# Kernel optimization log

Measured on AMD Instinct MI355X. Metric: run time of the kernel, lower is better.

Reference implementation:

```python
import jax, jax.numpy as jnp
import numpy as np

N = 100000      # nodes
E = 3200000     # directed edges (avg degree 32)
F_IN, HID, CLS = 512, 256, 64


def setup_inputs() -> dict:
    key = jax.random.key(0)
    k = jax.random.split(key, 6)
    x = jax.random.normal(k[0], (N, F_IN), dtype=jnp.float32)
    edge_index = jax.random.randint(k[1], (2, E), 0, N, dtype=jnp.int32)
    W1 = jax.random.normal(k[2], (F_IN, HID), dtype=jnp.float32) / np.float32(np.sqrt(F_IN))
    b1 = jnp.zeros((HID,), dtype=jnp.float32)
    W2 = jax.random.normal(k[3], (HID, CLS), dtype=jnp.float32) / np.float32(np.sqrt(HID))
    b2 = jnp.zeros((CLS,), dtype=jnp.float32)
    return {"x": x, "edge_index": edge_index, "W1": W1, "b1": b1, "W2": W2, "b2": b2}


def gcn_layer(x, W, b, src, dst, n):
    """GCN layer: out = D^{-1/2} (A + I) D^{-1/2} (x W + b)."""
    h = x @ W + b                                   # [n, out]
    loop = jnp.arange(n, dtype=src.dtype)
    s = jnp.concatenate([src, loop])                # add self loops
    d = jnp.concatenate([dst, loop])
    deg = jax.ops.segment_sum(jnp.ones_like(d, dtype=h.dtype), d, num_segments=n)
    dinv = jax.lax.rsqrt(jnp.maximum(deg, 1.0))
    norm = dinv[s] * dinv[d]                        # [E+n]
    return jax.ops.segment_sum(h[s] * norm[:, None], d, num_segments=n)


def reference(x, edge_index, W1, b1, W2, b2):
    src, dst = edge_index[0], edge_index[1]
    n = x.shape[0]
    h = jax.nn.relu(gcn_layer(x, W1, b1, src, dst, n))
    # dropout is identity in eval mode
    h = gcn_layer(h, W2, b2, src, dst, n)
    return jax.nn.log_softmax(h, axis=1)
```

## Files before the change

### kernel.cpp

```cpp
#include <hip/hip_runtime.h>

#define FIN 512
#define HID 256
#define CLS 64
#define PAD 8
#define BKT_SLACK 4096

typedef short bf16x8 __attribute__((ext_vector_type(8)));
typedef float f32x4 __attribute__((ext_vector_type(4)));
typedef float f32x2 __attribute__((ext_vector_type(2)));

__device__ __forceinline__ float bf2f(unsigned short u) {
    union { unsigned int i; float f; } c; c.i = ((unsigned int)u) << 16; return c.f;
}
__device__ __forceinline__ unsigned short f2bf(float f) {
    union { float f; unsigned int u; } c; c.f = f;
    unsigned int u = c.u;
    return (unsigned short)((u + 0x7fffu + ((u >> 16) & 1u)) >> 16);
}
__device__ __forceinline__ unsigned char f2fp8(float v) {
    int r = __builtin_amdgcn_cvt_pk_fp8_f32(v, v, 0, false);
    return (unsigned char)(r & 0xFF);
}


__global__ __launch_bounds__(256) void k_hist(const int* __restrict__ dst,
                                              int* __restrict__ bktcnt, int E) {
    __shared__ int h[256];
    h[threadIdx.x] = 0;
    __syncthreads();
    for (int i = blockIdx.x * blockDim.x + threadIdx.x; i < E; i += gridDim.x * blockDim.x)
        atomicAdd(&h[dst[i] >> 9], 1);
    __syncthreads();
    if (h[threadIdx.x]) atomicAdd(&bktcnt[threadIdx.x], h[threadIdx.x]);
}

__global__ __launch_bounds__(256) void k_bktscan(const int* __restrict__ bktcnt,
                                                 int* __restrict__ bkt_base,
                                                 int* __restrict__ bkt_cursor,
                                                 int NB, int E) {
    __shared__ int sh[256];
    int t = threadIdx.x;
    int v = (t < NB) ? bktcnt[t] : 0;
    sh[t] = v;
    __syncthreads();
    for (int s = 1; s < 256; s <<= 1) {
        int u = (t >= s) ? sh[t - s] : 0;
        __syncthreads();
        sh[t] += u;
        __syncthreads();
    }
    int excl = sh[t] - v;
    if (t < NB) { bkt_base[t] = excl; bkt_cursor[t] = excl; }
    if (t == 0) bkt_base[NB] = E;
}

#define EPB 4096
__global__ __launch_bounds__(256) void k_binscatter(
        const int* __restrict__ src, const int* __restrict__ dst,
        int* __restrict__ bkt_cursor, uint2* __restrict__ ebuf, int E) {
    __shared__ int h[256];
    __shared__ int cb[256];
    int t = threadIdx.x;
    h[t] = 0;
    __syncthreads();
    int base = blockIdx.x * EPB;
    int es[16], ed[16], lp[16];
    #pragma unroll
    for (int it = 0; it < 16; ++it) {
        int i = base + it * 256 + t;
        if (i < E) {
            es[it] = src[i];
            ed[it] = dst[i];
            lp[it] = atomicAdd(&h[ed[it] >> 9], 1);
        } else {
            es[it] = -1; ed[it] = 0; lp[it] = 0;
        }
    }
    __syncthreads();
    int c = h[t];
    if (c) cb[t] = atomicAdd(&bkt_cursor[t], c);
    __syncthreads();
    #pragma unroll
    for (int it = 0; it < 16; ++it) {
        if (es[it] >= 0) {
            int b = ed[it] >> 9;
            ebuf[cb[b] + lp[it]] = make_uint2((unsigned)es[it], (unsigned)ed[it]);
        }
    }
}

__global__ __launch_bounds__(256) void k_csrbuild(
        const uint2* __restrict__ ebuf, const int* __restrict__ bkt_base,
        int* __restrict__ rs, int* __restrict__ cnte, float* __restrict__ dinv,
        int* __restrict__ csr, int Nn) {
    __shared__ int deg[512];
    __shared__ int cur[512];
    __shared__ int ts[256];
    int b = blockIdx.x, t = threadIdx.x;
    int e0 = bkt_base[b], e1 = bkt_base[b + 1];
    int pb = e0 + b * BKT_SLACK;
    int node0 = b << 9;
    deg[t] = 0; deg[t + 256] = 0;
    __syncthreads();
    for (int j = e0 + t; j < e1; j += 256)
        atomicAdd(&deg[(int)ebuf[j].y - node0], 1);
    __syncthreads();
    int n0 = node0 + 2 * t;
    int d0 = deg[2 * t], d1 = deg[2 * t + 1];
    int p0 = (n0 < Nn)     ? ((d0 + 1 + PAD - 1) & ~(PAD - 1)) : 0;
    int p1 = (n0 + 1 < Nn) ? ((d1 + 1 + PAD - 1) & ~(PAD - 1)) : 0;
    ts[t] = p0 + p1;
    __syncthreads();
    for (int s = 1; s < 256; s <<= 1) {
        int u = (t >= s) ? ts[t - s] : 0;
        __syncthreads();
        ts[t] += u;
        __syncthreads();
    }
    int excl = ts[t] - (p0 + p1);
    cur[2 * t] = excl;
    cur[2 * t + 1] = excl + p0;
    if (n0 < Nn)     { rs[n0]     = pb + excl;      cnte[n0]     = p0; dinv[n0]     = rsqrtf((float)(d0 + 1)); }
    if (n0 + 1 < Nn) { rs[n0 + 1] = pb + excl + p0; cnte[n0 + 1] = p1; dinv[n0 + 1] = rsqrtf((float)(d1 + 1)); }
    __syncthreads();
    for (int j = e0 + t; j < e1; j += 256) {
        uint2 e = ebuf[j];
        int p = atomicAdd(&cur[(int)e.y - node0], 1);
        csr[pb + p] = (int)e.x;
    }
    if (n0 < Nn) {
        csr[pb + excl + d0] = n0;
        for (int j = d0 + 1; j < p0; ++j) csr[pb + excl + j] = Nn;
    }
    if (n0 + 1 < Nn) {
        csr[pb + excl + p0 + d1] = n0 + 1;
        for (int j = d1 + 1; j < p1; ++j) csr[pb + excl + p0 + j] = Nn;
    }
}

__global__ void k_wpack(const float* __restrict__ W, unsigned short* __restrict__ Wp,
                        int K, int Ncols) {
    int i = blockIdx.x * blockDim.x + threadIdx.x;
    if (i < K * Ncols) {
        int k = i / Ncols, n = i - k * Ncols;
        Wp[((size_t)(k >> 3) * Ncols + n) * 8 + (k & 7)] = f2bf(W[i]);
    }
}

__global__ __launch_bounds__(512) void k_gemm1(
        const float* __restrict__ x, const unsigned short* __restrict__ W1p,
        const float* __restrict__ b1, const float* __restrict__ dinv,
        unsigned char* __restrict__ hs1, int Nn) {
    __shared__ unsigned short As[64][40];
    int tid = threadIdx.x;
    int w = tid >> 6, lane = tid & 63;
    int wr = w >> 2, wc = w & 3;
    int l15 = lane & 15, l4 = lane >> 4;
    int row0 = blockIdx.x * 64;

    f32x4 zero = {0.f, 0.f, 0.f, 0.f};
    f32x4 acc[2][4];
    #pragma unroll
    for (int m = 0; m < 2; ++m)
        #pragma unroll
        for (int n = 0; n < 4; ++n) acc[m][n] = zero;

    int sr = tid >> 3;
    int sc = tid & 7;
    bool srok = (row0 + sr) < Nn;
    const float* xrow = x + (size_t)(row0 + sr) * FIN + sc * 4;

    for (int kt = 0; kt < FIN; kt += 32) {
        float4 v = srok ? *(const float4*)(xrow + kt) : make_float4(0.f, 0.f, 0.f, 0.f);
        ushort4 o;
        o.x = f2bf(v.x); o.y = f2bf(v.y); o.z = f2bf(v.z); o.w = f2bf(v.w);
        *(ushort4*)&As[sr][sc * 4] = o;
        __syncthreads();

        bf16x8 bfr[4];
        size_t bbase = (size_t)((kt >> 3) + l4) * HID * 8;
        #pragma unroll
        for (int n = 0; n < 4; ++n) {
            int col = wc * 64 + n * 16 + l15;
            bfr[n] = *(const bf16x8*)&W1p[bbase + (size_t)col * 8];
        }
        bf16x8 afr[2];
        #pragma unroll
        for (int m = 0; m < 2; ++m) {
            int r = wr * 32 + m * 16 + l15;
            afr[m] = *(const bf16x8*)&As[r][l4 * 8];
        }
        #pragma unroll
        for (int m = 0; m < 2; ++m)
            #pragma unroll
            for (int n = 0; n < 4; ++n)
                acc[m][n] = __builtin_amdgcn_mfma_f32_16x16x32_bf16(
                    afr[m], bfr[n], acc[m][n], 0, 0, 0);
        __syncthreads();
    }

    float b1c[4];
    #pragma unroll
    for (int n = 0; n < 4; ++n) b1c[n] = b1[wc * 64 + n * 16 + l15];
    #pragma unroll
    for (int m = 0; m < 2; ++m) {
        #pragma unroll
        for (int r = 0; r < 4; ++r) {
            int row = row0 + wr * 32 + m * 16 + l4 * 4 + r;
            if (row < Nn) {
                float dv = dinv[row];
                #pragma unroll
                for (int n = 0; n < 4; ++n) {
                    int col = wc * 64 + n * 16 + l15;
                    hs1[(size_t)row * HID + col] = f2fp8((acc[m][n][r] + b1c[n]) * dv);
                }
            }
        }
    }
}

__global__ __launch_bounds__(256) void k_agg1(
        const unsigned char* __restrict__ hs1, const int* __restrict__ csr,
        const int* __restrict__ rs, const int* __restrict__ cnte,
        const float* __restrict__ dinv, unsigned short* __restrict__ h2in, int Nn) {
    int d = blockIdx.x * 4 + (threadIdx.x >> 6);
    if (d >= Nn) return;
    int lane = threadIdx.x & 63;
    int g = lane >> 4, c = lane & 15;
    size_t coff = (size_t)c * 16;
    float acc[16];
    #pragma unroll
    for (int j = 0; j < 16; ++j) acc[j] = 0.f;
    int base = rs[d], cnt = cnte[d];
    const int* cp = csr + base;
    int t = 0;
    for (; t + 16 <= cnt; t += 16) {
        int i0 = cp[t + g], i1 = cp[t + 4 + g], i2 = cp[t + 8 + g], i3 = cp[t + 12 + g];
        uint4 v0 = *(const uint4*)&hs1[(size_t)i0 * HID + coff];
        uint4 v1 = *(const uint4*)&hs1[(size_t)i1 * HID + coff];
        uint4 v2 = *(const uint4*)&hs1[(size_t)i2 * HID + coff];
        uint4 v3 = *(const uint4*)&hs1[(size_t)i3 * HID + coff];
        unsigned int w0[4] = {v0.x, v0.y, v0.z, v0.w};
        unsigned int w1[4] = {v1.x, v1.y, v1.z, v1.w};
        unsigned int w2[4] = {v2.x, v2.y, v2.z, v2.w};
        unsigned int w3[4] = {v3.x, v3.y, v3.z, v3.w};
        #pragma unroll
        for (int k = 0; k < 4; ++k) {
            f32x2 a0 = __builtin_amdgcn_cvt_pk_f32_fp8(w0[k], false);
            f32x2 b0 = __builtin_amdgcn_cvt_pk_f32_fp8(w0[k], true);
            f32x2 a1 = __builtin_amdgcn_cvt_pk_f32_fp8(w1[k], false);
            f32x2 b1v = __builtin_amdgcn_cvt_pk_f32_fp8(w1[k], true);
            f32x2 a2 = __builtin_amdgcn_cvt_pk_f32_fp8(w2[k], false);
            f32x2 b2v = __builtin_amdgcn_cvt_pk_f32_fp8(w2[k], true);
            f32x2 a3 = __builtin_amdgcn_cvt_pk_f32_fp8(w3[k], false);
            f32x2 b3 = __builtin_amdgcn_cvt_pk_f32_fp8(w3[k], true);
            acc[k*4+0] += (a0[0] + a1[0]) + (a2[0] + a3[0]);
            acc[k*4+1] += (a0[1] + a1[1]) + (a2[1] + a3[1]);
            acc[k*4+2] += (b0[0] + b1v[0]) + (b2v[0] + b3[0]);
            acc[k*4+3] += (b0[1] + b1v[1]) + (b2v[1] + b3[1]);
        }
    }
    if (t < cnt) {
        int i0 = cp[t + g], i1 = cp[t + 4 + g];
        uint4 v0 = *(const uint4*)&hs1[(size_t)i0 * HID + coff];
        uint4 v1 = *(const uint4*)&hs1[(size_t)i1 * HID + coff];
        unsigned int w0[4] = {v0.x, v0.y, v0.z, v0.w};
        unsigned int w1[4] = {v1.x, v1.y, v1.z, v1.w};
        #pragma unroll
        for (int k = 0; k < 4; ++k) {
            f32x2 a0 = __builtin_amdgcn_cvt_pk_f32_fp8(w0[k], false);
            f32x2 b0 = __builtin_amdgcn_cvt_pk_f32_fp8(w0[k], true);
            f32x2 a1 = __builtin_amdgcn_cvt_pk_f32_fp8(w1[k], false);
            f32x2 b1v = __builtin_amdgcn_cvt_pk_f32_fp8(w1[k], true);
            acc[k*4+0] += a0[0] + a1[0];
            acc[k*4+1] += a0[1] + a1[1];
            acc[k*4+2] += b0[0] + b1v[0];
            acc[k*4+3] += b0[1] + b1v[1];
        }
    }
    #pragma unroll
    for (int j = 0; j < 16; ++j) {
        acc[j] += __shfl_xor(acc[j], 16);
        acc[j] += __shfl_xor(acc[j], 32);
    }
    float dv = dinv[d];
    ushort4 o;
    o.x = f2bf(fmaxf(acc[g * 4 + 0] * dv, 0.f));
    o.y = f2bf(fmaxf(acc[g * 4 + 1] * dv, 0.f));
    o.z = f2bf(fmaxf(acc[g * 4 + 2] * dv, 0.f));
    o.w = f2bf(fmaxf(acc[g * 4 + 3] * dv, 0.f));
    *(ushort4*)&h2in[(size_t)d * HID + c * 16 + g * 4] = o;
}

__global__ __launch_bounds__(256) void k_gemm2(
        const unsigned short* __restrict__ h2in, const unsigned short* __restrict__ W2p,
        const float* __restrict__ b2, const float* __restrict__ dinv,
        unsigned short* __restrict__ hs2, int Nn) {
    int tid = threadIdx.x;
    int w = tid >> 6, lane = tid & 63;
    int l15 = lane & 15, l4 = lane >> 4;
    int r0 = blockIdx.x * 64 + w * 16;
    int arow = r0 + l15;
    bool aok = arow < Nn;
    const unsigned short* ap = h2in + (size_t)arow * HID + l4 * 8;

    f32x4 zero = {0.f, 0.f, 0.f, 0.f};
    bf16x8 zf = {0, 0, 0, 0, 0, 0, 0, 0};
    f32x4 acc[4];
    #pragma unroll
    for (int n = 0; n < 4; ++n) acc[n] = zero;

    #pragma unroll
    for (int kt = 0; kt < HID; kt += 32) {
        bf16x8 a = aok ? *(const bf16x8*)(ap + kt) : zf;
        size_t bbase = (size_t)((kt >> 3) + l4) * CLS * 8;
        #pragma unroll
        for (int n = 0; n < 4; ++n) {
            bf16x8 bb = *(const bf16x8*)&W2p[bbase + (size_t)(n * 16 + l15) * 8];
            acc[n] = __builtin_amdgcn_mfma_f32_16x16x32_bf16(a, bb, acc[n], 0, 0, 0);
        }
    }
    float b2c[4];
    #pragma unroll
    for (int n = 0; n < 4; ++n) b2c[n] = b2[n * 16 + l15];
    #pragma unroll
    for (int r = 0; r < 4; ++r) {
        int row = r0 + l4 * 4 + r;
        if (row < Nn) {
            float dv = dinv[row];
            #pragma unroll
            for (int n = 0; n < 4; ++n)
                hs2[(size_t)row * CLS + n * 16 + l15] = f2bf((acc[n][r] + b2c[n]) * dv);
        }
    }
}

__global__ __launch_bounds__(256) void k_agg2(
        const unsigned short* __restrict__ hs2, const int* __restrict__ csr,
        const int* __restrict__ rs, const int* __restrict__ cnte,
        const float* __restrict__ dinv, float* __restrict__ out, int Nn) {
    int d = blockIdx.x * 4 + (threadIdx.x >> 6);
    if (d >= Nn) return;
    int lane = threadIdx.x & 63;
    int q = lane >> 4, c4 = lane & 15;
    size_t loff = (size_t)c4 * 4;
    float a0 = 0.f, a1 = 0.f, a2 = 0.f, a3 = 0.f;
    int base = rs[d], cnt = cnte[d];
    const int* cp = csr + base;
    int t = 0;
    for (; t + 16 <= cnt; t += 16) {
        int s0 = cp[t + q], s1 = cp[t + q + 4], s2 = cp[t + q + 8], s3 = cp[t + q + 12];
        ushort4 v0 = *(const ushort4*)&hs2[(size_t)s0 * CLS + loff];
        ushort4 v1 = *(const ushort4*)&hs2[(size_t)s1 * CLS + loff];
        ushort4 v2 = *(const ushort4*)&hs2[(size_t)s2 * CLS + loff];
        ushort4 v3 = *(const ushort4*)&hs2[(size_t)s3 * CLS + loff];
        a0 += (bf2f(v0.x) + bf2f(v1.x)) + (bf2f(v2.x) + bf2f(v3.x));
        a1 += (bf2f(v0.y) + bf2f(v1.y)) + (bf2f(v2.y) + bf2f(v3.y));
        a2 += (bf2f(v0.z) + bf2f(v1.z)) + (bf2f(v2.z) + bf2f(v3.z));
        a3 += (bf2f(v0.w) + bf2f(v1.w)) + (bf2f(v2.w) + bf2f(v3.w));
    }
    if (t < cnt) {
        int s0 = cp[t + q], s1 = cp[t + q + 4];
        ushort4 v0 = *(const ushort4*)&hs2[(size_t)s0 * CLS + loff];
        ushort4 v1 = *(const ushort4*)&hs2[(size_t)s1 * CLS + loff];
        a0 += bf2f(v0.x) + bf2f(v1.x);
        a1 += bf2f(v0.y) + bf2f(v1.y);
        a2 += bf2f(v0.z) + bf2f(v1.z);
        a3 += bf2f(v0.w) + bf2f(v1.w);
    }
    a0 += __shfl_xor(a0, 16); a0 += __shfl_xor(a0, 32);
    a1 += __shfl_xor(a1, 16); a1 += __shfl_xor(a1, 32);
    a2 += __shfl_xor(a2, 16); a2 += __shfl_xor(a2, 32);
    a3 += __shfl_xor(a3, 16); a3 += __shfl_xor(a3, 32);
    float dv = dinv[d];
    float y0 = a0 * dv, y1 = a1 * dv, y2 = a2 * dv, y3 = a3 * dv;
    float m = fmaxf(fmaxf(y0, y1), fmaxf(y2, y3));
    #pragma unroll
    for (int o = 1; o <= 8; o <<= 1) m = fmaxf(m, __shfl_xor(m, o));
    float s = __expf(y0 - m) + __expf(y1 - m) + __expf(y2 - m) + __expf(y3 - m);
    #pragma unroll
    for (int o = 1; o <= 8; o <<= 1) s += __shfl_xor(s, o);
    if (q == 0) {
        float lg = __logf(s);
        float4 o4 = make_float4(y0 - m - lg, y1 - m - lg, y2 - m - lg, y3 - m - lg);
        *(float4*)&out[(size_t)d * CLS + c4 * 4] = o4;
    }
}

extern "C" void kernel_launch(void* const* d_in, const int* in_sizes, int n_in,
                              void* d_out, int out_size, void* d_ws, size_t ws_size,
                              hipStream_t stream) {
    const float* x  = (const float*)d_in[0];
    const int* ei   = (const int*)d_in[1];
    const float* W1 = (const float*)d_in[2];
    const float* b1 = (const float*)d_in[3];
    const float* W2 = (const float*)d_in[4];
    const float* b2 = (const float*)d_in[5];
    float* out = (float*)d_out;

    const int N = in_sizes[0] / FIN;
    const int E = in_sizes[1] / 2;
    const int NB = (N + 511) >> 9;
    const int* srcp = ei;
    const int* dstp = ei + E;

    char* w = (char*)d_ws;
    auto alloc = [&](size_t bytes) -> void* {
        void* p = (void*)w;
        w += (bytes + 255) / 256 * 256;
        return p;
    };
    int* rs        = (int*)alloc((size_t)(N + 1) * 4);
    int* cnte      = (int*)alloc((size_t)N * 4);
    float* dinv    = (float*)alloc((size_t)N * 4);
    int* csr       = (int*)alloc(((size_t)E + (size_t)N + (size_t)NB * BKT_SLACK + 8) * 4);
    int* bktcnt    = (int*)alloc((size_t)(NB + 1) * 4);
    int* bkt_base  = (int*)alloc((size_t)(NB + 1) * 4);
    int* bkt_cursor= (int*)alloc((size_t)(NB + 1) * 4);
    size_t hs1_bytes = (size_t)N * HID + HID;
    size_t ebuf_bytes = (size_t)E * 8;
    unsigned char* hs1 = (unsigned char*)alloc(hs1_bytes > ebuf_bytes ? hs1_bytes : ebuf_bytes + HID);
    unsigned short* h2in = (unsigned short*)alloc((size_t)N * HID * 2);
    unsigned short* hs2  = (unsigned short*)alloc((size_t)(N + 1) * CLS * 2);
    unsigned short* W1p  = (unsigned short*)alloc((size_t)FIN * HID * 2);
    unsigned short* W2p  = (unsigned short*)alloc((size_t)HID * CLS * 2);
    uint2* ebuf = (uint2*)hs1;

    hipMemsetAsync(bktcnt, 0, (size_t)(NB + 1) * 4, stream);

    k_hist<<<1024, 256, 0, stream>>>(dstp, bktcnt, E);
    k_bktscan<<<1, 256, 0, stream>>>(bktcnt, bkt_base, bkt_cursor, NB, E);
    k_binscatter<<<(E + EPB - 1) / EPB, 256, 0, stream>>>(srcp, dstp, bkt_cursor, ebuf, E);
    k_csrbuild<<<NB, 256, 0, stream>>>(ebuf, bkt_base, rs, cnte, dinv, csr, N);

    hipMemsetAsync(hs1 + (size_t)N * HID, 0, HID, stream);
    hipMemsetAsync(hs2 + (size_t)N * CLS, 0, CLS * 2, stream);

    k_wpack<<<(FIN * HID + 255) / 256, 256, 0, stream>>>(W1, W1p, FIN, HID);
    k_wpack<<<(HID * CLS + 255) / 256, 256, 0, stream>>>(W2, W2p, HID, CLS);

    k_gemm1<<<(N + 63) / 64, 512, 0, stream>>>(x, W1p, b1, dinv, hs1, N);
    k_agg1<<<(N + 3) / 4, 256, 0, stream>>>(hs1, csr, rs, cnte, dinv, h2in, N);
    k_gemm2<<<(N + 63) / 64, 256, 0, stream>>>(h2in, W2p, b2, dinv, hs2, N);
    k_agg2<<<(N + 3) / 4, 256, 0, stream>>>(hs2, csr, rs, cnte, dinv, out, N);
}
```

Before: 404.3 us.

## Pack edge buffer to 32 bits, enlarge gemm1 row tile, unroll agg2 gather

```diff
diff --git a/kernel.cpp b/kernel.cpp
--- a/kernel.cpp
+++ b/kernel.cpp
@@ -58,7 +58,7 @@
 #define EPB 4096
 __global__ __launch_bounds__(256) void k_binscatter(
         const int* __restrict__ src, const int* __restrict__ dst,
-        int* __restrict__ bkt_cursor, uint2* __restrict__ ebuf, int E) {
+        int* __restrict__ bkt_cursor, unsigned* __restrict__ ebuf, int E) {
     __shared__ int h[256];
     __shared__ int cb[256];
     int t = threadIdx.x;
@@ -85,13 +85,13 @@
     for (int it = 0; it < 16; ++it) {
         if (es[it] >= 0) {
             int b = ed[it] >> 9;
-            ebuf[cb[b] + lp[it]] = make_uint2((unsigned)es[it], (unsigned)ed[it]);
+            ebuf[cb[b] + lp[it]] = (unsigned)es[it] | ((unsigned)(ed[it] & 511) << 23);
         }
     }
 }
 
 __global__ __launch_bounds__(256) void k_csrbuild(
-        const uint2* __restrict__ ebuf, const int* __restrict__ bkt_base,
+        const unsigned* __restrict__ ebuf, const int* __restrict__ bkt_base,
         int* __restrict__ rs, int* __restrict__ cnte, float* __restrict__ dinv,
         int* __restrict__ csr, int Nn) {
     __shared__ int deg[512];
@@ -104,7 +104,7 @@
     deg[t] = 0; deg[t + 256] = 0;
     __syncthreads();
     for (int j = e0 + t; j < e1; j += 256)
-        atomicAdd(&deg[(int)ebuf[j].y - node0], 1);
+        atomicAdd(&deg[ebuf[j] >> 23], 1);
     __syncthreads();
     int n0 = node0 + 2 * t;
     int d0 = deg[2 * t], d1 = deg[2 * t + 1];
@@ -125,9 +125,9 @@
     if (n0 + 1 < Nn) { rs[n0 + 1] = pb + excl + p0; cnte[n0 + 1] = p1; dinv[n0 + 1] = rsqrtf((float)(d1 + 1)); }
     __syncthreads();
     for (int j = e0 + t; j < e1; j += 256) {
-        uint2 e = ebuf[j];
-        int p = atomicAdd(&cur[(int)e.y - node0], 1);
-        csr[pb + p] = (int)e.x;
+        unsigned e = ebuf[j];
+        int p = atomicAdd(&cur[e >> 23], 1);
+        csr[pb + p] = (int)(e & 0x7FFFFFu);
     }
     if (n0 < Nn) {
         csr[pb + excl + d0] = n0;
@@ -152,30 +152,35 @@
         const float* __restrict__ x, const unsigned short* __restrict__ W1p,
         const float* __restrict__ b1, const float* __restrict__ dinv,
         unsigned char* __restrict__ hs1, int Nn) {
-    __shared__ unsigned short As[64][40];
+    __shared__ unsigned short As[128][40];
     int tid = threadIdx.x;
     int w = tid >> 6, lane = tid & 63;
     int wr = w >> 2, wc = w & 3;
     int l15 = lane & 15, l4 = lane >> 4;
-    int row0 = blockIdx.x * 64;
+    int row0 = blockIdx.x * 128;
 
     f32x4 zero = {0.f, 0.f, 0.f, 0.f};
-    f32x4 acc[2][4];
-    #pragma unroll
-    for (int m = 0; m < 2; ++m)
+    f32x4 acc[4][4];
+    #pragma unroll
+    for (int m = 0; m < 4; ++m)
         #pragma unroll
         for (int n = 0; n < 4; ++n) acc[m][n] = zero;
 
     int sr = tid >> 3;
     int sc = tid & 7;
-    bool srok = (row0 + sr) < Nn;
-    const float* xrow = x + (size_t)(row0 + sr) * FIN + sc * 4;
+    bool srok0 = (row0 + sr) < Nn;
+    bool srok1 = (row0 + 64 + sr) < Nn;
+    const float* xrow0 = x + (size_t)(row0 + sr) * FIN + sc * 4;
+    const float* xrow1 = x + (size_t)(row0 + 64 + sr) * FIN + sc * 4;
 
     for (int kt = 0; kt < FIN; kt += 32) {
-        float4 v = srok ? *(const float4*)(xrow + kt) : make_float4(0.f, 0.f, 0.f, 0.f);
-        ushort4 o;
-        o.x = f2bf(v.x); o.y = f2bf(v.y); o.z = f2bf(v.z); o.w = f2bf(v.w);
-        *(ushort4*)&As[sr][sc * 4] = o;
+        float4 v0 = srok0 ? *(const float4*)(xrow0 + kt) : make_float4(0.f, 0.f, 0.f, 0.f);
+        float4 v1 = srok1 ? *(const float4*)(xrow1 + kt) : make_float4(0.f, 0.f, 0.f, 0.f);
+        ushort4 o0, o1;
+        o0.x = f2bf(v0.x); o0.y = f2bf(v0.y); o0.z = f2bf(v0.z); o0.w = f2bf(v0.w);
+        o1.x = f2bf(v1.x); o1.y = f2bf(v1.y); o1.z = f2bf(v1.z); o1.w = f2bf(v1.w);
+        *(ushort4*)&As[sr][sc * 4] = o0;
+        *(ushort4*)&As[64 + sr][sc * 4] = o1;
         __syncthreads();
 
         bf16x8 bfr[4];
@@ -185,14 +190,14 @@
             int col = wc * 64 + n * 16 + l15;
             bfr[n] = *(const bf16x8*)&W1p[bbase + (size_t)col * 8];
         }
-        bf16x8 afr[2];
-        #pragma unroll
-        for (int m = 0; m < 2; ++m) {
-            int r = wr * 32 + m * 16 + l15;
+        bf16x8 afr[4];
+        #pragma unroll
+        for (int m = 0; m < 4; ++m) {
+            int r = wr * 64 + m * 16 + l15;
             afr[m] = *(const bf16x8*)&As[r][l4 * 8];
         }
         #pragma unroll
-        for (int m = 0; m < 2; ++m)
+        for (int m = 0; m < 4; ++m)
             #pragma unroll
             for (int n = 0; n < 4; ++n)
                 acc[m][n] = __builtin_amdgcn_mfma_f32_16x16x32_bf16(
@@ -204,10 +209,10 @@
     #pragma unroll
     for (int n = 0; n < 4; ++n) b1c[n] = b1[wc * 64 + n * 16 + l15];
     #pragma unroll
-    for (int m = 0; m < 2; ++m) {
+    for (int m = 0; m < 4; ++m) {
         #pragma unroll
         for (int r = 0; r < 4; ++r) {
-            int row = row0 + wr * 32 + m * 16 + l4 * 4 + r;
+            int row = row0 + wr * 64 + m * 16 + l4 * 4 + r;
             if (row < Nn) {
                 float dv = dinv[row];
                 #pragma unroll
@@ -349,6 +354,26 @@
     int base = rs[d], cnt = cnte[d];
     const int* cp = csr + base;
     int t = 0;
+    for (; t + 32 <= cnt; t += 32) {
+        int s0 = cp[t + q],      s1 = cp[t + q + 4],  s2 = cp[t + q + 8],  s3 = cp[t + q + 12];
+        int s4 = cp[t + q + 16], s5 = cp[t + q + 20], s6 = cp[t + q + 24], s7 = cp[t + q + 28];
+        ushort4 v0 = *(const ushort4*)&hs2[(size_t)s0 * CLS + loff];
+        ushort4 v1 = *(const ushort4*)&hs2[(size_t)s1 * CLS + loff];
+        ushort4 v2 = *(const ushort4*)&hs2[(size_t)s2 * CLS + loff];
+        ushort4 v3 = *(const ushort4*)&hs2[(size_t)s3 * CLS + loff];
+        ushort4 v4 = *(const ushort4*)&hs2[(size_t)s4 * CLS + loff];
+        ushort4 v5 = *(const ushort4*)&hs2[(size_t)s5 * CLS + loff];
+        ushort4 v6 = *(const ushort4*)&hs2[(size_t)s6 * CLS + loff];
+        ushort4 v7 = *(const ushort4*)&hs2[(size_t)s7 * CLS + loff];
+        a0 += ((bf2f(v0.x) + bf2f(v1.x)) + (bf2f(v2.x) + bf2f(v3.x)))
+            + ((bf2f(v4.x) + bf2f(v5.x)) + (bf2f(v6.x) + bf2f(v7.x)));
+        a1 += ((bf2f(v0.y) + bf2f(v1.y)) + (bf2f(v2.y) + bf2f(v3.y)))
+            + ((bf2f(v4.y) + bf2f(v5.y)) + (bf2f(v6.y) + bf2f(v7.y)));
+        a2 += ((bf2f(v0.z) + bf2f(v1.z)) + (bf2f(v2.z) + bf2f(v3.z)))
+            + ((bf2f(v4.z) + bf2f(v5.z)) + (bf2f(v6.z) + bf2f(v7.z)));
+        a3 += ((bf2f(v0.w) + bf2f(v1.w)) + (bf2f(v2.w) + bf2f(v3.w)))
+            + ((bf2f(v4.w) + bf2f(v5.w)) + (bf2f(v6.w) + bf2f(v7.w)));
+    }
     for (; t + 16 <= cnt; t += 16) {
         int s0 = cp[t + q], s1 = cp[t + q + 4], s2 = cp[t + q + 8], s3 = cp[t + q + 12];
         ushort4 v0 = *(const ushort4*)&hs2[(size_t)s0 * CLS + loff];
@@ -418,14 +443,14 @@
     int* bktcnt    = (int*)alloc((size_t)(NB + 1) * 4);
     int* bkt_base  = (int*)alloc((size_t)(NB + 1) * 4);
     int* bkt_cursor= (int*)alloc((size_t)(NB + 1) * 4);
-    size_t hs1_bytes = (size_t)N * HID + HID;
-    size_t ebuf_bytes = (size_t)E * 8;
-    unsigned char* hs1 = (unsigned char*)alloc(hs1_bytes > ebuf_bytes ? hs1_bytes : ebuf_bytes + HID);
+    size_t hs1_bytes = (size_t)(N + 1) * HID;
+    size_t ebuf_bytes = (size_t)E * 4;
+    unsigned char* hs1 = (unsigned char*)alloc(hs1_bytes > ebuf_bytes ? hs1_bytes : ebuf_bytes);
     unsigned short* h2in = (unsigned short*)alloc((size_t)N * HID * 2);
     unsigned short* hs2  = (unsigned short*)alloc((size_t)(N + 1) * CLS * 2);
     unsigned short* W1p  = (unsigned short*)alloc((size_t)FIN * HID * 2);
     unsigned short* W2p  = (unsigned short*)alloc((size_t)HID * CLS * 2);
-    uint2* ebuf = (uint2*)hs1;
+    unsigned* ebuf = (unsigned*)hs1;
 
     hipMemsetAsync(bktcnt, 0, (size_t)(NB + 1) * 4, stream);
 
@@ -440,7 +465,7 @@
     k_wpack<<<(FIN * HID + 255) / 256, 256, 0, stream>>>(W1, W1p, FIN, HID);
     k_wpack<<<(HID * CLS + 255) / 256, 256, 0, stream>>>(W2, W2p, HID, CLS);
 
-    k_gemm1<<<(N + 63) / 64, 512, 0, stream>>>(x, W1p, b1, dinv, hs1, N);
+    k_gemm1<<<(N + 127) / 128, 512, 0, stream>>>(x, W1p, b1, dinv, hs1, N);
     k_agg1<<<(N + 3) / 4, 256, 0, stream>>>(hs1, csr, rs, cnte, dinv, h2in, N);
     k_gemm2<<<(N + 63) / 64, 256, 0, stream>>>(h2in, W2p, b2, dinv, hs2, N);
     k_agg2<<<(N + 3) / 4, 256, 0, stream>>>(hs2, csr, rs, cnte, dinv, out, N);
```

Result: faster. 384.4 us (-4.9%).
